# Performance work log

Measured on AMD Instinct MI355X. Metric: run time of the kernel, lower is better.

## Reference

```python
import jax, jax.numpy as jnp
import numpy as np

EPS = 1e-5
H, D = 8, 64  # n_heads, head_n_channels


def _instance_norm(x):
    # x: [B, H, N, D]; InstanceNorm1d over grid axis N per (batch, head, channel)
    m = jnp.mean(x, axis=2, keepdims=True)
    v = jnp.var(x, axis=2, keepdims=True)
    return (x - m) * jax.lax.rsqrt(v + EPS)


def setup_inputs() -> dict:
    key = jax.random.key(0)
    ks = jax.random.split(key, 7)
    B, N, C, OUT = 4, 16384, 256, 256
    u_src = jax.random.normal(ks[0], (B, N, C), jnp.float32)
    pos_src = jax.random.uniform(ks[1], (B, N, 2), jnp.float32)
    s_in = 1.0 / np.sqrt(C)
    Wq = jax.random.normal(ks[2], (H * D, C), jnp.float32) * s_in
    Wk = jax.random.normal(ks[3], (H * D, C), jnp.float32) * s_in
    Wv = jax.random.normal(ks[4], (H * D, C), jnp.float32) * s_in
    Wo = jax.random.normal(ks[5], (OUT, H * D), jnp.float32) * (1.0 / np.sqrt(H * D))
    bo = jnp.zeros((OUT,), jnp.float32)
    return {"u_src": u_src, "pos_src": pos_src, "Wq": Wq, "Wk": Wk, "Wv": Wv, "Wo": Wo, "bo": bo}


def reference(u_src, pos_src, Wq, Wk, Wv, Wo, bo):
    B, N, C = u_src.shape
    # q/k/v projections -> [B, H, N, D]
    q = (u_src @ Wq.T).reshape(B, N, H, D).transpose(0, 2, 1, 3)
    k = (u_src @ Wk.T).reshape(B, N, H, D).transpose(0, 2, 1, 3)
    v = (u_src @ Wv.T).reshape(B, N, H, D).transpose(0, 2, 1, 3)
    # instance-norm k, v over the grid (domain) axis
    k = _instance_norm(k)
    v = _instance_norm(v)
    # associative linear attention with uniform quadrature weights 1/N
    w = 1.0 / N
    kv = jnp.einsum('bhnd,bhne->bhde', k, v * w)   # [B,H,D,D]
    u = jnp.einsum('bhnd,bhde->bhne', q, kv)       # [B,H,N,D]
    u = u.transpose(0, 2, 1, 3).reshape(B, N, H * D)
    return u @ Wo.T + bo
```

## Files before the change

kernel.cpp:

```cpp
#include <hip/hip_runtime.h>
#include <hip/hip_bf16.h>

#define BB    4
#define NTOT  16384
#define CC    256
#define HH    8
#define DD    64
#define HD    512
#define OUTC  256

typedef unsigned short u16;
typedef unsigned int u32;
typedef __attribute__((ext_vector_type(8))) short bf16x8;
typedef __attribute__((ext_vector_type(4))) float f32x4;
typedef __attribute__((ext_vector_type(4))) short u16x4;
typedef __attribute__((ext_vector_type(4))) u32 u32x4;

__device__ __forceinline__ float b2f(u16 u) {
    union { float f; u32 i; } x; x.i = ((u32)u) << 16; return x.f;
}
__device__ __forceinline__ u16 f2b(float f) {
    union { float f; u32 i; } x; x.f = f;
    u32 r = x.i + 0x7fffu + ((x.i >> 16) & 1u);
    return (u16)(r >> 16);
}

#define GLD(gp, lp) __builtin_amdgcn_global_load_lds( \
    (const __attribute__((address_space(1))) void*)(gp), \
    (__attribute__((address_space(3))) void*)(lp), 16, 0, 0)

#define MFMA(a, b, c) __builtin_amdgcn_mfma_f32_16x16x32_bf16((a), (b), (c), 0, 0, 0)

__global__ __launch_bounds__(256) void wcvt(
    const float* __restrict__ Wq, const float* __restrict__ Wk,
    const float* __restrict__ Wv, const float* __restrict__ Wo,
    u16* __restrict__ q, u16* __restrict__ k,
    u16* __restrict__ v, u16* __restrict__ o)
{
    const int z = blockIdx.z;
    const float* src = z == 0 ? Wq : z == 1 ? Wk : z == 2 ? Wv : Wo;
    u16* dst = z == 0 ? q : z == 1 ? k : z == 2 ? v : o;
    const int i = (blockIdx.x * 256 + threadIdx.x) * 8;
    const float4 a = *(const float4*)(src + i);
    const float4 b = *(const float4*)(src + i + 4);
    union { bf16x8 v; u16 s[8]; } w;
    w.s[0] = f2b(a.x); w.s[1] = f2b(a.y); w.s[2] = f2b(a.z); w.s[3] = f2b(a.w);
    w.s[4] = f2b(b.x); w.s[5] = f2b(b.y); w.s[6] = f2b(b.z); w.s[7] = f2b(b.w);
    *(bf16x8*)(dst + i) = w.v;
}

__global__ __launch_bounds__(512) void ggemm(
    const float* __restrict__ u, float* __restrict__ Gp, float* __restrict__ suP)
{
    __shared__ u32 Ts[16 * 290];
    const int z = blockIdx.x, b = z >> 6, ck = z & 63;
    const float* base = u + (long long)b * NTOT * CC + (long long)ck * 256 * CC;
    const int t = threadIdx.x, w = t >> 6, l = t & 63;
    const int wy = w >> 1, wx = w & 1;
    const int r16 = l & 15, quad = l >> 4;
    const int sp = t >> 5;
    const int sq = t & 31;

    const int csa0 = 9 * ((wy * 64 + r16) >> 3) + (r16 & 7);
    const int csb0 = 9 * ((wx * 128 + r16) >> 3) + (r16 & 7);
    const int pr0 = 4 * quad * 290;

    f32x4 acc[4][8] = {};
    float su = 0.f;

    float4 a0, a1, b0, b1;
    {
        const float* src = base + (long long)(2 * sp) * CC + sq * 8;
        a0 = *(const float4*)src;       a1 = *(const float4*)(src + 4);
        b0 = *(const float4*)(src + CC); b1 = *(const float4*)(src + CC + 4);
    }

    for (int it = 0; it < 8; it++) {
        __syncthreads();
        {
            u32 pk[8];
            pk[0] = (u32)(u16)f2b(a0.x) | ((u32)f2b(b0.x) << 16);
            pk[1] = (u32)(u16)f2b(a0.y) | ((u32)f2b(b0.y) << 16);
            pk[2] = (u32)(u16)f2b(a0.z) | ((u32)f2b(b0.z) << 16);
            pk[3] = (u32)(u16)f2b(a0.w) | ((u32)f2b(b0.w) << 16);
            pk[4] = (u32)(u16)f2b(a1.x) | ((u32)f2b(b1.x) << 16);
            pk[5] = (u32)(u16)f2b(a1.y) | ((u32)f2b(b1.y) << 16);
            pk[6] = (u32)(u16)f2b(a1.z) | ((u32)f2b(b1.z) << 16);
            pk[7] = (u32)(u16)f2b(a1.w) | ((u32)f2b(b1.w) << 16);
            u32* dst = Ts + sp * 290 + 9 * sq;
#pragma unroll
            for (int k = 0; k < 8; k++) dst[k] = pk[k];
        }
        if (it < 7) {
            const float* src = base + (long long)((it + 1) * 32 + 2 * sp) * CC + sq * 8;
            a0 = *(const float4*)src;       a1 = *(const float4*)(src + 4);
            b0 = *(const float4*)(src + CC); b1 = *(const float4*)(src + CC + 4);
        }
        __syncthreads();

        if (t < 256) {
            const int cs = 9 * (t >> 3) + (t & 7);
            float s1 = 0.f;
#pragma unroll
            for (int p = 0; p < 16; p++) {
                u32 v = Ts[p * 290 + cs];
                s1 += b2f((u16)(v & 0xffff)) + b2f((u16)(v >> 16));
            }
            su += s1;
        }

        bf16x8 a[4], bb[8];
#pragma unroll
        for (int i = 0; i < 4; i++) {
            const int cs = csa0 + 18 * i;
            union { u32x4 u4; bf16x8 h; } f;
            f.u4[0] = Ts[pr0 + cs];       f.u4[1] = Ts[pr0 + 290 + cs];
            f.u4[2] = Ts[pr0 + 580 + cs]; f.u4[3] = Ts[pr0 + 870 + cs];
            a[i] = f.h;
        }
#pragma unroll
        for (int j = 0; j < 8; j++) {
            const int cs = csb0 + 18 * j;
            union { u32x4 u4; bf16x8 h; } f;
            f.u4[0] = Ts[pr0 + cs];       f.u4[1] = Ts[pr0 + 290 + cs];
            f.u4[2] = Ts[pr0 + 580 + cs]; f.u4[3] = Ts[pr0 + 870 + cs];
            bb[j] = f.h;
        }
#pragma unroll
        for (int i = 0; i < 4; i++)
#pragma unroll
            for (int j = 0; j < 8; j++)
                acc[i][j] = MFMA(a[i], bb[j], acc[i][j]);
    }

    float* Cp = Gp + (long long)z * 65536;
#pragma unroll
    for (int i = 0; i < 4; i++)
#pragma unroll
        for (int j = 0; j < 8; j++)
#pragma unroll
            for (int rr = 0; rr < 4; rr++)
                Cp[(wy * 64 + 16 * i + quad * 4 + rr) * 256 + wx * 128 + 16 * j + r16]
                    = acc[i][j][rr];
    if (t < 256) suP[z * 256 + t] = su;
}

__global__ __launch_bounds__(256) void gred(
    const float* __restrict__ Gp, const float* __restrict__ suP,
    u16* __restrict__ Gb, float* __restrict__ su)
{
    const int b = blockIdx.y, t = threadIdx.x;
    const int row = blockIdx.x * 4 + (t >> 6);
    const int col = (t & 63) * 4;
    const float* p = Gp + (long long)(b * 64) * 65536 + row * 256 + col;
    f32x4 s = {};
#pragma unroll
    for (int ck = 0; ck < 64; ck++) {
        f32x4 v = *(const f32x4*)(p + (long long)ck * 65536);
        s[0] += v[0]; s[1] += v[1]; s[2] += v[2]; s[3] += v[3];
    }
    union { u16x4 v; u16 q[4]; } pk;
#pragma unroll
    for (int k = 0; k < 4; k++) pk.q[k] = f2b(s[k]);
    *(u16x4*)(Gb + (long long)b * 65536 + row * 256 + col) = pk.v;

    if (blockIdx.x == 0) {
        float s2 = 0.f;
#pragma unroll
        for (int ck = 0; ck < 64; ck++) s2 += suP[(b * 64 + ck) * 256 + t];
        su[b * 256 + t] = s2;
    }
}

__global__ __launch_bounds__(256) void midend(
    const u16* __restrict__ Gb, const float* __restrict__ su,
    const u16* __restrict__ Wk_b, const u16* __restrict__ Wv_b,
    const u16* __restrict__ Wq_b, u16* __restrict__ Zt)
{
    __shared__ u16 pool[20480];
    __shared__ float e2kL[64], e2vL[64], mkL[64], rkL[64], mvL[64], rvL[64];

    const int bx = blockIdx.x, b = bx >> 3, h = bx & 7;
    const int t = threadIdx.x, w = t >> 6, l = t & 63;
    const int r16 = l & 15, quad = l >> 4;

    const u16* WkH = Wk_b + (h * 64) * 256;
    const u16* WvH = Wv_b + (h * 64) * 256;
    const u16* GbB = Gb + (long long)b * 65536;

    if (t < 64) e2kL[t] = 0.f;
    else if (t < 128) e2vL[t - 64] = 0.f;

    f32x4 acck[4][4] = {}, accv[4][4] = {};
    for (int ch = 0; ch < 8; ch++) {
        const int kk = ch * 32 + quad * 8;
        bf16x8 ak[4], av[4], bg[4];
#pragma unroll
        for (int i = 0; i < 4; i++) {
            ak[i] = *(const bf16x8*)(WkH + (16 * i + r16) * 256 + kk);
            av[i] = *(const bf16x8*)(WvH + (16 * i + r16) * 256 + kk);
        }
#pragma unroll
        for (int j = 0; j < 4; j++)
            bg[j] = *(const bf16x8*)(GbB + (w * 64 + 16 * j + r16) * 256 + kk);
#pragma unroll
        for (int i = 0; i < 4; i++)
#pragma unroll
            for (int j = 0; j < 4; j++) {
                acck[i][j] = MFMA(ak[i], bg[j], acck[i][j]);
                accv[i][j] = MFMA(av[i], bg[j], accv[i][j]);
            }
    }
    __syncthreads();

    u16* PkL = pool;
#pragma unroll
    for (int i = 0; i < 4; i++) {
#pragma unroll
        for (int rr = 0; rr < 4; rr++) {
            const int a = 16 * i + quad * 4 + rr;
            float e2k = 0.f, e2v = 0.f;
#pragma unroll
            for (int jt = 0; jt < 4; jt++) {
                const int j = w * 64 + 16 * jt + r16;
                PkL[(j >> 5) * 2048 + a * 32 + (j & 31)] = f2b(acck[i][jt][rr]);
                e2k += acck[i][jt][rr] * b2f(WkH[a * 256 + j]);
                e2v += accv[i][jt][rr] * b2f(WvH[a * 256 + j]);
            }
            atomicAdd(&e2kL[a], e2k);
            atomicAdd(&e2vL[a], e2v);
        }
    }
    __syncthreads();

    if (t < 128) {
        const int a = t & 63;
        const u16* Wrow = (t < 64) ? (WkH + a * 256) : (WvH + a * 256);
        const float* suB = su + b * 256;
        float m = 0.f;
        for (int c8 = 0; c8 < 32; c8++) {
            bf16x8 wr = *(const bf16x8*)(Wrow + c8 * 8);
#pragma unroll
            for (int k = 0; k < 8; k++) m += b2f((u16)wr[k]) * suB[c8 * 8 + k];
        }
        m *= (1.0f / NTOT);
        const float e2 = ((t < 64) ? e2kL[a] : e2vL[a]) * (1.0f / NTOT);
        const float r = rsqrtf(e2 - m * m + 1e-5f);
        if (t < 64) { mkL[a] = m; rkL[a] = r; }
        else        { mvL[a] = m; rvL[a] = r; }
    }
    __syncthreads();

    const int mh = (w >> 1) * 32, nh = (w & 1) * 32;
    float mkR[2][4], rkR[2][4], mvR[2], rvR[2];
#pragma unroll
    for (int i = 0; i < 2; i++)
#pragma unroll
        for (int rr = 0; rr < 4; rr++) {
            mkR[i][rr] = mkL[mh + 16 * i + quad * 4 + rr];
            rkR[i][rr] = rkL[mh + 16 * i + quad * 4 + rr];
        }
#pragma unroll
    for (int j = 0; j < 2; j++) {
        mvR[j] = mvL[nh + 16 * j + r16];
        rvR[j] = rvL[nh + 16 * j + r16];
    }

    f32x4 accs[2][2] = {};
    for (int ch = 0; ch < 8; ch++) {
        const int ko = quad * 8;
        bf16x8 ap[2], bv[2];
#pragma unroll
        for (int i = 0; i < 2; i++)
            ap[i] = *(const bf16x8*)(PkL + ch * 2048 + (mh + 16 * i + r16) * 32 + ko);
#pragma unroll
        for (int j = 0; j < 2; j++)
            bv[j] = *(const bf16x8*)(WvH + (nh + 16 * j + r16) * 256 + ch * 32 + ko);
#pragma unroll
        for (int i = 0; i < 2; i++)
#pragma unroll
            for (int j = 0; j < 2; j++)
                accs[i][j] = MFMA(ap[i], bv[j], accs[i][j]);
    }
    __syncthreads();

    u16* kvTL = pool;
    u16* WqTL = pool + 4096;
#pragma unroll
    for (int i = 0; i < 2; i++)
#pragma unroll
        for (int j = 0; j < 2; j++)
#pragma unroll
            for (int rr = 0; rr < 4; rr++) {
                const int d = mh + 16 * i + quad * 4 + rr;
                const int e = nh + 16 * j + r16;
                const float kv = rkR[i][rr] * rvR[j] *
                    (accs[i][j][rr] * (1.0f / NTOT) - mkR[i][rr] * mvR[j]);
                kvTL[(d >> 5) * 2048 + e * 32 + (d & 31)] = f2b(kv);
            }
    {
        const int d = t >> 2, q = t & 3;
        const u16* Wrow = Wq_b + (h * 64 + d) * 256 + q * 64;
#pragma unroll
        for (int s = 0; s < 8; s++) {
            bf16x8 raw = *(const bf16x8*)(Wrow + s * 8);
#pragma unroll
            for (int k = 0; k < 8; k++) {
                const int c = q * 64 + s * 8 + k;
                WqTL[(d >> 5) * 8192 + c * 32 + (d & 31)] = (u16)raw[k];
            }
        }
    }
    __syncthreads();

    f32x4 accy[4][4] = {};
#pragma unroll
    for (int ch = 0; ch < 2; ch++) {
        const int ko = quad * 8;
        bf16x8 akv[4], bq[4];
#pragma unroll
        for (int i = 0; i < 4; i++)
            akv[i] = *(const bf16x8*)(kvTL + ch * 2048 + (16 * i + r16) * 32 + ko);
#pragma unroll
        for (int j = 0; j < 4; j++)
            bq[j] = *(const bf16x8*)(WqTL + ch * 8192 + (w * 64 + 16 * j + r16) * 32 + ko);
#pragma unroll
        for (int i = 0; i < 4; i++)
#pragma unroll
            for (int j = 0; j < 4; j++)
                accy[i][j] = MFMA(akv[i], bq[j], accy[i][j]);
    }
#pragma unroll
    for (int i = 0; i < 4; i++)
#pragma unroll
        for (int j = 0; j < 4; j++) {
            const int c = w * 64 + 16 * j + r16;
            const int e0 = 16 * i + quad * 4;
            union { u16x4 v; u16 s[4]; } pk;
#pragma unroll
            for (int rr = 0; rr < 4; rr++) pk.s[rr] = f2b(accy[i][j][rr]);
            *(u16x4*)(Zt + ((long long)(b * 256 + c)) * 512 + h * 64 + e0) = pk.v;
        }
}

template <typename CT>
__global__ __launch_bounds__(256) void gemm_bt(
    const u16* __restrict__ A, const u16* __restrict__ Bm,
    CT* __restrict__ C, const float* __restrict__ bias,
    int K, int lda, int ldc,
    long long aStride, long long bStride, long long cStride)
{
    __shared__ u16 As[128 * 32];
    __shared__ u16 Bs[128 * 32];

    const int bz = blockIdx.z;
    A  += (long long)bz * aStride;
    Bm += (long long)bz * bStride;
    C  += (long long)bz * cStride;

    const int m0 = blockIdx.x * 128;
    const int n0 = blockIdx.y * 128;
    const int t  = threadIdx.x;
    const int wv = t >> 6, l = t & 63;
    const int wy = wv >> 1, wx = wv & 1;
    const int r16  = l & 15;
    const int quad = l >> 4;
    const int srow = wv * 16 + (l >> 2);
    const int scol = (l & 3) * 8;

    f32x4 acc[4][4] = {};

    for (int kk = 0; kk < K; kk += 32) {
#pragma unroll
        for (int s = 0; s < 2; s++) {
            GLD(A + (long long)(m0 + s * 64 + srow) * lda + kk + scol,
                As + s * 2048 + wv * 512);
            GLD(Bm + (long long)(n0 + s * 64 + srow) * K + kk + scol,
                Bs + s * 2048 + wv * 512);
        }
        __syncthreads();

        bf16x8 a[4], b[4];
#pragma unroll
        for (int i = 0; i < 4; i++)
            a[i] = *(const bf16x8*)(As + (wy * 64 + 16 * i + r16) * 32 + quad * 8);
#pragma unroll
        for (int j = 0; j < 4; j++)
            b[j] = *(const bf16x8*)(Bs + (wx * 64 + 16 * j + r16) * 32 + quad * 8);
#pragma unroll
        for (int i = 0; i < 4; i++)
#pragma unroll
            for (int j = 0; j < 4; j++)
                acc[i][j] = MFMA(a[i], b[j], acc[i][j]);
        __syncthreads();
    }

#pragma unroll
    for (int j = 0; j < 4; j++) {
        const int col = n0 + wx * 64 + 16 * j + r16;
        const float bv = bias ? bias[col] : 0.0f;
#pragma unroll
        for (int i = 0; i < 4; i++) {
#pragma unroll
            for (int r = 0; r < 4; r++) {
                const int row = m0 + wy * 64 + 16 * i + quad * 4 + r;
                const float v = acc[i][j][r] + bv;
                if constexpr (sizeof(CT) == 2) C[(long long)row * ldc + col] = f2b(v);
                else                           C[(long long)row * ldc + col] = v;
            }
        }
    }
}

__global__ __launch_bounds__(256) void gemm_uf32(
    const float* __restrict__ uf, const u16* __restrict__ Ft,
    float* __restrict__ C, const float* __restrict__ bias)
{
    __shared__ u16 As[128 * 32];
    __shared__ u16 Bs[128 * 32];

    const int b = blockIdx.z;
    uf += (long long)b * NTOT * CC;
    const u16* Bm = Ft + (long long)b * 65536;
    C += (long long)b * NTOT * OUTC;

    const int m0 = blockIdx.x * 128;
    const int n0 = blockIdx.y * 128;
    const int t  = threadIdx.x;
    const int wv = t >> 6, l = t & 63;
    const int wy = wv >> 1, wx = wv & 1;
    const int r16  = l & 15;
    const int quad = l >> 4;
    const int srow = wv * 16 + (l >> 2);
    const int scol = (l & 3) * 8;
    const int ar = t >> 1, ah = t & 1;

    f32x4 acc[4][4] = {};

    for (int kk = 0; kk < 256; kk += 32) {
        {
            const float* s = uf + (long long)(m0 + ar) * CC + kk + ah * 16;
            float4 v0 = *(const float4*)s;
            float4 v1 = *(const float4*)(s + 4);
            float4 v2 = *(const float4*)(s + 8);
            float4 v3 = *(const float4*)(s + 12);
            union { bf16x8 v; u16 q[8]; } p0, p1;
            p0.q[0]=f2b(v0.x); p0.q[1]=f2b(v0.y); p0.q[2]=f2b(v0.z); p0.q[3]=f2b(v0.w);
            p0.q[4]=f2b(v1.x); p0.q[5]=f2b(v1.y); p0.q[6]=f2b(v1.z); p0.q[7]=f2b(v1.w);
            p1.q[0]=f2b(v2.x); p1.q[1]=f2b(v2.y); p1.q[2]=f2b(v2.z); p1.q[3]=f2b(v2.w);
            p1.q[4]=f2b(v3.x); p1.q[5]=f2b(v3.y); p1.q[6]=f2b(v3.z); p1.q[7]=f2b(v3.w);
            u16* d = As + ar * 32 + ah * 16;
            *(bf16x8*)d = p0.v;
            *(bf16x8*)(d + 8) = p1.v;
        }
#pragma unroll
        for (int s = 0; s < 2; s++)
            GLD(Bm + (long long)(n0 + s * 64 + srow) * 256 + kk + scol,
                Bs + s * 2048 + wv * 512);
        __syncthreads();

        bf16x8 a[4], bb[4];
#pragma unroll
        for (int i = 0; i < 4; i++)
            a[i] = *(const bf16x8*)(As + (wy * 64 + 16 * i + r16) * 32 + quad * 8);
#pragma unroll
        for (int j = 0; j < 4; j++)
            bb[j] = *(const bf16x8*)(Bs + (wx * 64 + 16 * j + r16) * 32 + quad * 8);
#pragma unroll
        for (int i = 0; i < 4; i++)
#pragma unroll
            for (int j = 0; j < 4; j++)
                acc[i][j] = MFMA(a[i], bb[j], acc[i][j]);
        __syncthreads();
    }

#pragma unroll
    for (int j = 0; j < 4; j++) {
        const int col = n0 + wx * 64 + 16 * j + r16;
        const float bv = bias[col];
#pragma unroll
        for (int i = 0; i < 4; i++) {
#pragma unroll
            for (int r = 0; r < 4; r++) {
                const int row = m0 + wy * 64 + 16 * i + quad * 4 + r;
                C[(long long)row * OUTC + col] = acc[i][j][r] + bv;
            }
        }
    }
}

extern "C" void kernel_launch(void* const* d_in, const int* in_sizes, int n_in,
                              void* d_out, int out_size, void* d_ws, size_t ws_size,
                              hipStream_t stream)
{
    const float* u_src = (const float*)d_in[0];
    const float* Wq = (const float*)d_in[2];
    const float* Wk = (const float*)d_in[3];
    const float* Wv = (const float*)d_in[4];
    const float* Wo = (const float*)d_in[5];
    const float* bo = (const float*)d_in[6];
    float* out = (float*)d_out;

    char* ws = (char*)d_ws;
    size_t off = 0;
    float* Gp  = (float*)(ws + off); off += 67108864;
    float* suP = (float*)(ws + off); off += 262144;
    u16*  Gb   = (u16*)(ws + off);  off += 524288;
    u16*  Wq_b = (u16*)(ws + off);  off += 262144;
    u16*  Wk_b = (u16*)(ws + off);  off += 262144;
    u16*  Wv_b = (u16*)(ws + off);  off += 262144;
    u16*  Wo_b = (u16*)(ws + off);  off += 262144;
    float* su  = (float*)(ws + off); off += 4096;
    u16*  Zt   = (u16*)(ws + off);  off += 1048576;
    u16*  Ft   = (u16*)(ws + off);  off += 524288;

    const dim3 blk(256);

    wcvt<<<dim3(64, 1, 4), blk, 0, stream>>>(Wq, Wk, Wv, Wo, Wq_b, Wk_b, Wv_b, Wo_b);

    ggemm<<<dim3(BB * 64), dim3(512), 0, stream>>>(u_src, Gp, suP);
    gred<<<dim3(64, BB), blk, 0, stream>>>(Gp, suP, Gb, su);

    midend<<<dim3(BB * HH), blk, 0, stream>>>(Gb, su, Wk_b, Wv_b, Wq_b, Zt);

    gemm_bt<u16><<<dim3(2, 2, BB), blk, 0, stream>>>(
        Wo_b, Zt, Ft, nullptr, 512, 512, 256, 0, 131072, 65536);

    gemm_uf32<<<dim3(128, 2, BB), blk, 0, stream>>>(u_src, Ft, out, bo);
}
```

Before: 221.9 us.

## Split midend Gram projection into parallel GEMM and widen final GEMM tile

The serial [Wk;Wv]·G projection inside the 32-block midend kernel moves to a separate gemm_bt launch over 64 blocks. It writes P2 to workspace, and the slimmed skvz kernel reads P2 back from global memory for the variance and kv computation. This spreads the heavy per-head MFMA work across more CUs, at the cost of an extra launch and a global round trip. Separately, the final u_src×Ft GEMM now covers all 256 output columns per block, so the fp32 u_src tile is loaded and converted once instead of twice, with more accumulator registers per thread.

```diff
diff --git a/kernel.cpp b/kernel.cpp
--- a/kernel.cpp
+++ b/kernel.cpp
@@ -172,13 +172,13 @@
     }
 }
 
-__global__ __launch_bounds__(256) void midend(
-    const u16* __restrict__ Gb, const float* __restrict__ su,
+__global__ __launch_bounds__(256) void skvz(
+    const u16* __restrict__ P2, const float* __restrict__ su,
     const u16* __restrict__ Wk_b, const u16* __restrict__ Wv_b,
     const u16* __restrict__ Wq_b, u16* __restrict__ Zt)
 {
     __shared__ u16 pool[20480];
-    __shared__ float e2kL[64], e2vL[64], mkL[64], rkL[64], mvL[64], rvL[64];
+    __shared__ float mkL[64], rkL[64], mvL[64], rvL[64];
 
     const int bx = blockIdx.x, b = bx >> 3, h = bx & 7;
     const int t = threadIdx.x, w = t >> 6, l = t & 63;
@@ -186,68 +186,34 @@
 
     const u16* WkH = Wk_b + (h * 64) * 256;
     const u16* WvH = Wv_b + (h * 64) * 256;
-    const u16* GbB = Gb + (long long)b * 65536;
-
-    if (t < 64) e2kL[t] = 0.f;
-    else if (t < 128) e2vL[t - 64] = 0.f;
-
-    f32x4 acck[4][4] = {}, accv[4][4] = {};
-    for (int ch = 0; ch < 8; ch++) {
-        const int kk = ch * 32 + quad * 8;
-        bf16x8 ak[4], av[4], bg[4];
-#pragma unroll
-        for (int i = 0; i < 4; i++) {
-            ak[i] = *(const bf16x8*)(WkH + (16 * i + r16) * 256 + kk);
-            av[i] = *(const bf16x8*)(WvH + (16 * i + r16) * 256 + kk);
-        }
-#pragma unroll
-        for (int j = 0; j < 4; j++)
-            bg[j] = *(const bf16x8*)(GbB + (w * 64 + 16 * j + r16) * 256 + kk);
-#pragma unroll
-        for (int i = 0; i < 4; i++)
-#pragma unroll
-            for (int j = 0; j < 4; j++) {
-                acck[i][j] = MFMA(ak[i], bg[j], acck[i][j]);
-                accv[i][j] = MFMA(av[i], bg[j], accv[i][j]);
-            }
-    }
-    __syncthreads();
-
-    u16* PkL = pool;
-#pragma unroll
-    for (int i = 0; i < 4; i++) {
-#pragma unroll
-        for (int rr = 0; rr < 4; rr++) {
-            const int a = 16 * i + quad * 4 + rr;
-            float e2k = 0.f, e2v = 0.f;
-#pragma unroll
-            for (int jt = 0; jt < 4; jt++) {
-                const int j = w * 64 + 16 * jt + r16;
-                PkL[(j >> 5) * 2048 + a * 32 + (j & 31)] = f2b(acck[i][jt][rr]);
-                e2k += acck[i][jt][rr] * b2f(WkH[a * 256 + j]);
-                e2v += accv[i][jt][rr] * b2f(WvH[a * 256 + j]);
-            }
-            atomicAdd(&e2kL[a], e2k);
-            atomicAdd(&e2vL[a], e2v);
-        }
-    }
-    __syncthreads();
-
-    if (t < 128) {
-        const int a = t & 63;
-        const u16* Wrow = (t < 64) ? (WkH + a * 256) : (WvH + a * 256);
-        const float* suB = su + b * 256;
-        float m = 0.f;
-        for (int c8 = 0; c8 < 32; c8++) {
-            bf16x8 wr = *(const bf16x8*)(Wrow + c8 * 8);
-#pragma unroll
-            for (int k = 0; k < 8; k++) m += b2f((u16)wr[k]) * suB[c8 * 8 + k];
-        }
-        m *= (1.0f / NTOT);
-        const float e2 = ((t < 64) ? e2kL[a] : e2vL[a]) * (1.0f / NTOT);
-        const float r = rsqrtf(e2 - m * m + 1e-5f);
-        if (t < 64) { mkL[a] = m; rkL[a] = r; }
-        else        { mvL[a] = m; rvL[a] = r; }
+    const u16* PkH = P2 + (long long)b * 262144 + (h * 64) * 256;
+    const u16* PvH = P2 + (long long)b * 262144 + (512 + h * 64) * 256;
+
+    {
+        const int row = t >> 1, half = t & 1;
+        const u16* Prow = (row < 64 ? PkH + row * 256 : PvH + (row - 64) * 256) + half * 128;
+        const u16* Wrow = (row < 64 ? WkH + row * 256 : WvH + (row - 64) * 256) + half * 128;
+        const float* suB = su + b * 256 + half * 128;
+        float e2 = 0.f, m = 0.f;
+#pragma unroll
+        for (int c8 = 0; c8 < 16; c8++) {
+            bf16x8 pw = *(const bf16x8*)(Prow + c8 * 8);
+            bf16x8 ww = *(const bf16x8*)(Wrow + c8 * 8);
+#pragma unroll
+            for (int k = 0; k < 8; k++) {
+                const float wv_ = b2f((u16)ww[k]);
+                e2 += b2f((u16)pw[k]) * wv_;
+                m  += wv_ * suB[c8 * 8 + k];
+            }
+        }
+        e2 += __shfl_xor(e2, 1);
+        m  += __shfl_xor(m, 1);
+        if (half == 0) {
+            m *= (1.0f / NTOT);
+            const float r = rsqrtf(e2 * (1.0f / NTOT) - m * m + 1e-5f);
+            if (row < 64) { mkL[row] = m; rkL[row] = r; }
+            else          { mvL[row - 64] = m; rvL[row - 64] = r; }
+        }
     }
     __syncthreads();
 
@@ -272,7 +238,7 @@
         bf16x8 ap[2], bv[2];
 #pragma unroll
         for (int i = 0; i < 2; i++)
-            ap[i] = *(const bf16x8*)(PkL + ch * 2048 + (mh + 16 * i + r16) * 32 + ko);
+            ap[i] = *(const bf16x8*)(PkH + (mh + 16 * i + r16) * 256 + ch * 32 + ko);
 #pragma unroll
         for (int j = 0; j < 2; j++)
             bv[j] = *(const bf16x8*)(WvH + (nh + 16 * j + r16) * 256 + ch * 32 + ko);
@@ -282,7 +248,6 @@
             for (int j = 0; j < 2; j++)
                 accs[i][j] = MFMA(ap[i], bv[j], accs[i][j]);
     }
-    __syncthreads();
 
     u16* kvTL = pool;
     u16* WqTL = pool + 4096;
@@ -412,12 +377,12 @@
     }
 }
 
-__global__ __launch_bounds__(256) void gemm_uf32(
+__global__ __launch_bounds__(256) void gemm_uf32w(
     const float* __restrict__ uf, const u16* __restrict__ Ft,
     float* __restrict__ C, const float* __restrict__ bias)
 {
     __shared__ u16 As[128 * 32];
-    __shared__ u16 Bs[128 * 32];
+    __shared__ u16 Bs[256 * 32];
 
     const int b = blockIdx.z;
     uf += (long long)b * NTOT * CC;
@@ -425,7 +390,6 @@
     C += (long long)b * NTOT * OUTC;
 
     const int m0 = blockIdx.x * 128;
-    const int n0 = blockIdx.y * 128;
     const int t  = threadIdx.x;
     const int wv = t >> 6, l = t & 63;
     const int wy = wv >> 1, wx = wv & 1;
@@ -435,7 +399,7 @@
     const int scol = (l & 3) * 8;
     const int ar = t >> 1, ah = t & 1;
 
-    f32x4 acc[4][4] = {};
+    f32x4 acc[4][8] = {};
 
     for (int kk = 0; kk < 256; kk += 32) {
         {
@@ -454,29 +418,29 @@
             *(bf16x8*)(d + 8) = p1.v;
         }
 #pragma unroll
-        for (int s = 0; s < 2; s++)
-            GLD(Bm + (long long)(n0 + s * 64 + srow) * 256 + kk + scol,
+        for (int s = 0; s < 4; s++)
+            GLD(Bm + (long long)(s * 64 + srow) * 256 + kk + scol,
                 Bs + s * 2048 + wv * 512);
         __syncthreads();
 
-        bf16x8 a[4], bb[4];
+        bf16x8 a[4], bb[8];
 #pragma unroll
         for (int i = 0; i < 4; i++)
             a[i] = *(const bf16x8*)(As + (wy * 64 + 16 * i + r16) * 32 + quad * 8);
 #pragma unroll
-        for (int j = 0; j < 4; j++)
-            bb[j] = *(const bf16x8*)(Bs + (wx * 64 + 16 * j + r16) * 32 + quad * 8);
-#pragma unroll
-        for (int i = 0; i < 4; i++)
-#pragma unroll
-            for (int j = 0; j < 4; j++)
+        for (int j = 0; j < 8; j++)
+            bb[j] = *(const bf16x8*)(Bs + (wx * 128 + 16 * j + r16) * 32 + quad * 8);
+#pragma unroll
+        for (int i = 0; i < 4; i++)
+#pragma unroll
+            for (int j = 0; j < 8; j++)
                 acc[i][j] = MFMA(a[i], bb[j], acc[i][j]);
         __syncthreads();
     }
 
 #pragma unroll
-    for (int j = 0; j < 4; j++) {
-        const int col = n0 + wx * 64 + 16 * j + r16;
+    for (int j = 0; j < 8; j++) {
+        const int col = wx * 128 + 16 * j + r16;
         const float bv = bias[col];
 #pragma unroll
         for (int i = 0; i < 4; i++) {
@@ -513,6 +477,7 @@
     float* su  = (float*)(ws + off); off += 4096;
     u16*  Zt   = (u16*)(ws + off);  off += 1048576;
     u16*  Ft   = (u16*)(ws + off);  off += 524288;
+    u16*  P2   = (u16*)(ws + off);  off += 2097152;
 
     const dim3 blk(256);
 
@@ -521,10 +486,13 @@
     ggemm<<<dim3(BB * 64), dim3(512), 0, stream>>>(u_src, Gp, suP);
     gred<<<dim3(64, BB), blk, 0, stream>>>(Gp, suP, Gb, su);
 
-    midend<<<dim3(BB * HH), blk, 0, stream>>>(Gb, su, Wk_b, Wv_b, Wq_b, Zt);
+    gemm_bt<u16><<<dim3(8, 2, BB), blk, 0, stream>>>(
+        Wk_b, Gb, P2, nullptr, 256, 256, 256, 0, 65536, 262144);
+
+    skvz<<<dim3(BB * HH), blk, 0, stream>>>(P2, su, Wk_b, Wv_b, Wq_b, Zt);
 
     gemm_bt<u16><<<dim3(2, 2, BB), blk, 0, stream>>>(
         Wo_b, Zt, Ft, nullptr, 512, 512, 256, 0, 131072, 65536);
 
-    gemm_uf32<<<dim3(128, 2, BB), blk, 0, stream>>>(u_src, Ft, out, bo);
-}
+    gemm_uf32w<<<dim3(128, 1, BB), blk, 0, stream>>>(u_src, Ft, out, bo);
+}
```

Result: faster. 211.1 us (-4.9%).
